# Kernel tuning notes

Measured on AMD Instinct MI355X. Metric: run time of the kernel, lower is better.

The kernel has to match this reference:

```python
import jax, jax.numpy as jnp
import numpy as np

INF = 1000000000.0
D = 1024


def setup_inputs() -> dict:
    key = jax.random.key(0)
    k_enc, k_r = jax.random.split(key)
    encoding = jax.random.normal(k_enc, (8, 2048, D), dtype=jnp.float32)
    R = jax.random.normal(k_r, (D, D), dtype=jnp.float32) / D  # init_with_zeros=False
    return {"encoding": encoding, "R": R}


def reference(encoding, R):
    b, n, d = encoding.shape
    # Q = encoding @ R ; scores = Q @ encoding^T  (bilinear relation attention)
    encR = jnp.einsum("bnd,de->bne", encoding, R)          # [b, n, d]
    scores = jnp.einsum("bnd,bmd->bnm", encR, encoding)     # [b, n, n]
    # causal mask: -INF above the diagonal (use_mask=True)
    mask = jnp.where(jnp.tril(jnp.ones((n, n), dtype=bool)), 0.0, -INF).astype(scores.dtype)
    A = jax.nn.softmax(scores + mask, axis=2)               # [b, n, n]
    return jnp.einsum("bnm,bmd->bnd", A, encoding)          # [b, n, d]
```

## Files before the change

### kernel.cpp

```cpp
#include <hip/hip_runtime.h>
#include <hip/hip_bf16.h>


typedef __attribute__((ext_vector_type(4))) float f32x4;
typedef __attribute__((ext_vector_type(4))) unsigned u32x4;
typedef __attribute__((ext_vector_type(8))) __fp16 f16x8;
typedef __attribute__((ext_vector_type(4))) __fp16 f16x4;
typedef __attribute__((ext_vector_type(2))) __fp16 f16x2;

#define MFMA16H(A, B, C) __builtin_amdgcn_mfma_f32_16x16x32_f16(A, B, C, 0, 0, 0)

__device__ __forceinline__ f16x4 cvt4h(f32x4 a) {
    union { f16x4 v; f16x2 h[2]; } r;
    r.h[0] = __builtin_amdgcn_cvt_pkrtz(a[0], a[1]);
    r.h[1] = __builtin_amdgcn_cvt_pkrtz(a[2], a[3]);
    return r.v;
}

__device__ __forceinline__ void gload16(const void* g, void* l) {
    __builtin_amdgcn_global_load_lds(
        (const __attribute__((address_space(1))) unsigned*)g,
        (__attribute__((address_space(3))) unsigned*)l, 16, 0, 0);
}

__global__ __launch_bounds__(256) void transpose_cvt_kernel(
    const float* __restrict__ src, __fp16* __restrict__ dstT,
    __fp16* __restrict__ dstH, int R, int C)
{
    __shared__ __align__(16) char lt[64 * 128];
    const int t = threadIdx.x;
    const int bz = blockIdx.z;
    const int r0 = blockIdx.x * 64, c0 = blockIdx.y * 64;
    const size_t so = (size_t)bz * R * C;
    const int tr = t >> 4;
    const int tc4 = (t & 15) * 4;
#pragma unroll
    for (int p = 0; p < 4; ++p) {
        int rl = tr + 16 * p;
        f32x4 x = *(const f32x4*)(src + so + (size_t)(r0 + rl) * C + c0 + tc4);
        f16x4 h = cvt4h(x);
        if (dstH) *(f16x4*)(dstH + so + (size_t)(r0 + rl) * C + c0 + tc4) = h;
        *(f16x4*)(lt + rl * 128 + ((tc4 * 2) ^ ((rl & 7) << 4))) = h;
    }
    __syncthreads();
#pragma unroll
    for (int p = 0; p < 4; ++p) {
        int dl = tr + 16 * p;
#pragma unroll
        for (int j = 0; j < 4; ++j) {
            int kl = (t & 15) + 16 * j;
            __fp16 v = *(const __fp16*)(lt + kl * 128 + ((dl * 2) ^ ((kl & 7) << 4)));
            dstT[so + (size_t)(c0 + dl) * R + r0 + kl] = v;
        }
    }
}

template <int CMODE>
__device__ __forceinline__ void gemm_core(
    const __fp16* __restrict__ A, const __fp16* __restrict__ B,
    char* __restrict__ Cptr, int ldA, int ldB, int ldC, int K, bool diag)
{
    __shared__ __align__(16) char sA[128 * 128];
    __shared__ __align__(16) char sB[128 * 128];
    const int t = threadIdx.x;
    const int w = t >> 6, l = t & 63;
    const int l15 = l & 15, lg = l >> 4;
    const int r0 = (w >> 1) * 64, c0 = (w & 1) * 64;
    const int swz = (l15 & 7) << 4;

    f32x4 acc[4][4];
#pragma unroll
    for (int i = 0; i < 4; ++i)
#pragma unroll
        for (int j = 0; j < 4; ++j) acc[i][j] = (f32x4){0.f, 0.f, 0.f, 0.f};

    const int strow = 32 * w + (l >> 3);
    const int gsrc = (((l & 7) ^ (l >> 3)) << 3);
    const __fp16* pa = A + (size_t)strow * ldA + gsrc;
    const __fp16* pb = B + (size_t)strow * ldB + gsrc;

    for (int kk = 0; kk < K; kk += 64) {
        __syncthreads();
#pragma unroll
        for (int i = 0; i < 4; ++i) {
            gload16(pa + (size_t)(8 * i) * ldA + kk, sA + w * 4096 + i * 1024);
            gload16(pb + (size_t)(8 * i) * ldB + kk, sB + w * 4096 + i * 1024);
        }
        __syncthreads();
#pragma unroll
        for (int ks = 0; ks < 2; ++ks) {
            f16x8 af[4], bf[4];
#pragma unroll
            for (int mt = 0; mt < 4; ++mt)
                af[mt] = *(const f16x8*)(sA + (r0 + 16 * mt + l15) * 128 + ((64 * ks + 16 * lg) ^ swz));
#pragma unroll
            for (int nt = 0; nt < 4; ++nt)
                bf[nt] = *(const f16x8*)(sB + (c0 + 16 * nt + l15) * 128 + ((64 * ks + 16 * lg) ^ swz));
#pragma unroll
            for (int mt = 0; mt < 4; ++mt)
#pragma unroll
                for (int nt = 0; nt < 4; ++nt)
                    acc[mt][nt] = MFMA16H(af[mt], bf[nt], acc[mt][nt]);
        }
    }
#pragma unroll
    for (int mt = 0; mt < 4; ++mt)
#pragma unroll
        for (int nt = 0; nt < 4; ++nt)
#pragma unroll
            for (int rg = 0; rg < 4; ++rg) {
                int rr = r0 + 16 * mt + 4 * lg + rg;
                int cc = c0 + 16 * nt + l15;
                float v = acc[mt][nt][rg];
                if (CMODE == 2) {
                    *(float*)(Cptr + ((size_t)rr * ldC + cc) * 4) = v;
                } else {
                    if (CMODE == 1 && diag && cc > rr) v = -30000.f;
                    *(__fp16*)(Cptr + ((size_t)rr * ldC + cc) * 2) = (__fp16)v;
                }
            }
}

__global__ __launch_bounds__(256) void gemm_qr(
    const __fp16* __restrict__ encH, const __fp16* __restrict__ Rt,
    __fp16* __restrict__ Qh)
{
    const int bm = ((int)blockIdx.x >> 3) * 128;
    const int bn = ((int)blockIdx.x & 7) * 128;
    gemm_core<0>(encH + (size_t)bm * 1024, Rt + (size_t)bn * 1024,
                 (char*)(Qh + (size_t)bm * 1024 + bn), 1024, 1024, 1024, 1024, false);
}

__global__ __launch_bounds__(256) void gemm_s(
    const __fp16* __restrict__ Qh, const __fp16* __restrict__ encH,
    __fp16* __restrict__ S)
{
    const int b = (int)blockIdx.x & 7;
    int rem = 135 - ((int)blockIdx.x >> 3);
    int qt = 0;
    while (rem > qt) { rem -= qt + 1; ++qt; }
    const int kt = rem;
    const size_t bo = (size_t)b * 2048 * 1024;
    const size_t so = (size_t)b * 2048 * 2048;
    gemm_core<1>(Qh + bo + (size_t)(qt * 128) * 1024,
                 encH + bo + (size_t)(kt * 128) * 1024,
                 (char*)(S + so + (size_t)(qt * 128) * 2048 + kt * 128),
                 1024, 1024, 2048, 1024, qt == kt);
}

__global__ __launch_bounds__(256) void gemm_pv(
    const __fp16* __restrict__ P, const __fp16* __restrict__ encT,
    float* __restrict__ out)
{
    const int b = (int)blockIdx.x & 7;
    const int r = (int)blockIdx.x >> 3;
    const int qtb = 15 - (r >> 3);
    const int dblk = r & 7;
    const size_t so = (size_t)b * 2048 * 2048;
    const size_t to = (size_t)b * 1024 * 2048;
    const int K = 128 * (qtb + 1);
    gemm_core<2>(P + so + (size_t)(qtb * 128) * 2048,
                 encT + to + (size_t)(dblk * 128) * 2048,
                 (char*)(out + (size_t)b * 2048 * 1024 + (size_t)(qtb * 128) * 1024 + dblk * 128),
                 2048, 2048, 1024, K, false);
}

__global__ __launch_bounds__(256) void softmax_kernel(__fp16* __restrict__ S)
{
    const int t = threadIdx.x;
    const int wv = t >> 6, l = t & 63;
    const int r = blockIdx.x * 4 + wv;
    const int b = blockIdx.y;
    __fp16* row = S + ((size_t)b * 2048 + r) * 2048;
    const int L = ((r >> 7) + 1) << 7;

    float v[4][8];
    float mx = -1e30f;
#pragma unroll
    for (int i = 0; i < 4; ++i) {
        int c0 = 8 * l + 512 * i;
        if (c0 < L) {
            f16x8 h = *reinterpret_cast<const f16x8*>(row + c0);
#pragma unroll
            for (int j = 0; j < 8; ++j) { v[i][j] = (float)h[j]; mx = fmaxf(mx, v[i][j]); }
        } else {
#pragma unroll
            for (int j = 0; j < 8; ++j) v[i][j] = -1e30f;
        }
    }
#pragma unroll
    for (int off = 1; off < 64; off <<= 1) mx = fmaxf(mx, __shfl_xor(mx, off));
    float sm = 0.f;
#pragma unroll
    for (int i = 0; i < 4; ++i)
#pragma unroll
        for (int j = 0; j < 8; ++j) { v[i][j] = __expf(v[i][j] - mx); sm += v[i][j]; }
#pragma unroll
    for (int off = 1; off < 64; off <<= 1) sm += __shfl_xor(sm, off);
    const float inv = 1.f / sm;
#pragma unroll
    for (int i = 0; i < 4; ++i) {
        int c0 = 8 * l + 512 * i;
        if (c0 < L) {
            union { f16x8 v8; f16x2 h[4]; } o;
#pragma unroll
            for (int j = 0; j < 4; ++j)
                o.h[j] = __builtin_amdgcn_cvt_pkrtz(v[i][2 * j] * inv, v[i][2 * j + 1] * inv);
            *reinterpret_cast<f16x8*>(row + c0) = o.v8;
        }
    }
}

__global__ __launch_bounds__(256) void qr_gemm_kernel(
    const float* __restrict__ A, const float* __restrict__ B, float* C)
{
    __shared__ __align__(16) char sA[128 * 64];
    __shared__ __align__(16) char sB[128 * 64];
    const int t = threadIdx.x;
    const int w = t >> 6, l = t & 63;
    const int l15 = l & 15, lg = l >> 4;
    const int bm = blockIdx.x * 128;
    const int bn = blockIdx.y * 128;

    f32x4 acc[4][4];
#pragma unroll
    for (int i = 0; i < 4; ++i)
#pragma unroll
        for (int j = 0; j < 4; ++j) acc[i][j] = (f32x4){0.f, 0.f, 0.f, 0.f};

    const int kq = 4 * (t & 7);
    const int i2 = t >> 3;

    for (int kk = 0; kk < 1024; kk += 32) {
#pragma unroll
        for (int it = 0; it < 4; ++it) {
            int m = i2 + 32 * it;
            f32x4 x = *reinterpret_cast<const f32x4*>(&A[(size_t)(bm + m) * 1024 + kk + kq]);
            *reinterpret_cast<f16x4*>(sA + m * 64 + ((2 * kq) ^ (((m >> 1) & 3) << 4))) = cvt4h(x);
        }
        {
            int n0 = 4 * i2;
            f32x4 x[4];
#pragma unroll
            for (int r = 0; r < 4; ++r)
                x[r] = *reinterpret_cast<const f32x4*>(&B[(size_t)(kk + kq + r) * 1024 + bn + n0]);
#pragma unroll
            for (int j = 0; j < 4; ++j) {
                int n = n0 + j;
                union { f16x4 v; f16x2 h[2]; } s;
                s.h[0] = __builtin_amdgcn_cvt_pkrtz(x[0][j], x[1][j]);
                s.h[1] = __builtin_amdgcn_cvt_pkrtz(x[2][j], x[3][j]);
                *reinterpret_cast<f16x4*>(sB + n * 64 + ((2 * kq) ^ (((n >> 1) & 3) << 4))) = s.v;
            }
        }
        __syncthreads();
        f16x8 af[4], bfv[4];
        const int r0 = (w >> 1) * 64, c0 = (w & 1) * 64;
#pragma unroll
        for (int mt = 0; mt < 4; ++mt) {
            int m = r0 + 16 * mt + l15;
            af[mt] = *reinterpret_cast<f16x8*>(sA + m * 64 + ((16 * lg) ^ (((m >> 1) & 3) << 4)));
        }
#pragma unroll
        for (int nt = 0; nt < 4; ++nt) {
            int n = c0 + 16 * nt + l15;
            bfv[nt] = *reinterpret_cast<f16x8*>(sB + n * 64 + ((16 * lg) ^ (((n >> 1) & 3) << 4)));
        }
#pragma unroll
        for (int mt = 0; mt < 4; ++mt)
#pragma unroll
            for (int nt = 0; nt < 4; ++nt)
                acc[mt][nt] = MFMA16H(af[mt], bfv[nt], acc[mt][nt]);
        __syncthreads();
    }
#pragma unroll
    for (int mt = 0; mt < 4; ++mt)
#pragma unroll
        for (int nt = 0; nt < 4; ++nt)
#pragma unroll
            for (int rg = 0; rg < 4; ++rg) {
                int row = bm + (w >> 1) * 64 + 16 * mt + 4 * lg + rg;
                int col = bn + (w & 1) * 64 + 16 * nt + l15;
                C[(size_t)row * 1024 + col] = acc[mt][nt][rg];
            }
}

__global__ __launch_bounds__(256) void s_gemm_kernel(
    const float* __restrict__ Q, const float* __restrict__ enc, __fp16* __restrict__ S)
{
    __shared__ __align__(16) char sA[128 * 64];
    __shared__ __align__(16) char sB[128 * 64];
    const int t = threadIdx.x;
    const int w = t >> 6, l = t & 63;
    const int l15 = l & 15, lg = l >> 4;

    int rem = 135 - (int)blockIdx.x;
    int qt = 0;
    while (rem > qt) { rem -= qt + 1; ++qt; }
    const int kt = rem;
    const int b = blockIdx.y;
    const float* Arow = Q + ((size_t)b * 2048 + qt * 128) * 1024;
    const float* Brow = enc + ((size_t)b * 2048 + kt * 128) * 1024;

    f32x4 acc[4][4];
#pragma unroll
    for (int i = 0; i < 4; ++i)
#pragma unroll
        for (int j = 0; j < 4; ++j) acc[i][j] = (f32x4){0.f, 0.f, 0.f, 0.f};

    const int kq = 4 * (t & 7);
    const int i2 = t >> 3;

    for (int kk = 0; kk < 1024; kk += 32) {
#pragma unroll
        for (int it = 0; it < 4; ++it) {
            int m = i2 + 32 * it;
            int sw = (2 * kq) ^ (((m >> 1) & 3) << 4);
            f32x4 xa = *reinterpret_cast<const f32x4*>(&Arow[(size_t)m * 1024 + kk + kq]);
            f32x4 xb = *reinterpret_cast<const f32x4*>(&Brow[(size_t)m * 1024 + kk + kq]);
            *reinterpret_cast<f16x4*>(sA + m * 64 + sw) = cvt4h(xa);
            *reinterpret_cast<f16x4*>(sB + m * 64 + sw) = cvt4h(xb);
        }
        __syncthreads();
        f16x8 af[4], bfv[4];
        const int r0 = (w >> 1) * 64, c0 = (w & 1) * 64;
#pragma unroll
        for (int mt = 0; mt < 4; ++mt) {
            int m = r0 + 16 * mt + l15;
            af[mt] = *reinterpret_cast<f16x8*>(sA + m * 64 + ((16 * lg) ^ (((m >> 1) & 3) << 4)));
        }
#pragma unroll
        for (int nt = 0; nt < 4; ++nt) {
            int n = c0 + 16 * nt + l15;
            bfv[nt] = *reinterpret_cast<f16x8*>(sB + n * 64 + ((16 * lg) ^ (((n >> 1) & 3) << 4)));
        }
#pragma unroll
        for (int mt = 0; mt < 4; ++mt)
#pragma unroll
            for (int nt = 0; nt < 4; ++nt)
                acc[mt][nt] = MFMA16H(af[mt], bfv[nt], acc[mt][nt]);
        __syncthreads();
    }
    const int r0 = (w >> 1) * 64, c0 = (w & 1) * 64;
#pragma unroll
    for (int mt = 0; mt < 4; ++mt)
#pragma unroll
        for (int nt = 0; nt < 4; ++nt)
#pragma unroll
            for (int rg = 0; rg < 4; ++rg) {
                int rt = r0 + 16 * mt + 4 * lg + rg;
                int ct = c0 + 16 * nt + l15;
                float v = acc[mt][nt][rg];
                if (kt == qt && ct > rt) v = -30000.f;
                S[((size_t)b * 2048 + qt * 128 + rt) * 2048 + kt * 128 + ct] = (__fp16)v;
            }
}

__global__ __launch_bounds__(512) void pv_gemm_kernel(
    const __fp16* __restrict__ P, const float* __restrict__ enc, float* __restrict__ out)
{
    __shared__ __align__(16) char sA[128 * 128];
    __shared__ __align__(16) char sB[128 * 128];
    const int t = threadIdx.x;
    const int w = t >> 6, l = t & 63;
    const int l15 = l & 15, lg = (l >> 4) & 3;
    const int wq = w >> 2, wdv = w & 3;
    const int qtb = 15 - (int)blockIdx.x;
    const int dblk = blockIdx.y;
    const int b = blockIdx.z;
    const int q0 = 128 * qtb;
    const int nkv = 128 * (qtb + 1);
    const __fp16* Pbase = P + ((size_t)b * 2048 + q0) * 2048;
    const float* Eb = enc + (size_t)b * 2048 * 1024;

    f32x4 acc[4][2];
#pragma unroll
    for (int i = 0; i < 4; ++i)
#pragma unroll
        for (int j = 0; j < 2; ++j) acc[i][j] = (f32x4){0.f, 0.f, 0.f, 0.f};

    const int ar = t >> 2, aseg = t & 3;
    const int ba = t >> 5, bdq = t & 31;

    for (int kv0 = 0; kv0 < nkv; kv0 += 64) {
        __syncthreads();
        {
            const __fp16* src = Pbase + (size_t)ar * 2048 + kv0 + 16 * aseg;
            u32x4 v0 = *reinterpret_cast<const u32x4*>(src);
            u32x4 v1 = *reinterpret_cast<const u32x4*>(src + 8);
            const int sw = (ar & 7) << 4;
            *reinterpret_cast<u32x4*>(sA + ar * 128 + ((32 * aseg) ^ sw)) = v0;
            *reinterpret_cast<u32x4*>(sA + ar * 128 + ((32 * aseg + 16) ^ sw)) = v1;
        }
        {
            const float* src = Eb + (size_t)(kv0 + 4 * ba) * 1024 + 128 * dblk + 4 * bdq;
            f32x4 x0 = *reinterpret_cast<const f32x4*>(src);
            f32x4 x1 = *reinterpret_cast<const f32x4*>(src + 1024);
            f32x4 x2 = *reinterpret_cast<const f32x4*>(src + 2048);
            f32x4 x3 = *reinterpret_cast<const f32x4*>(src + 3072);
#pragma unroll
            for (int j = 0; j < 4; ++j) {
                int d = 4 * bdq + j;
                union { f16x4 v; f16x2 h[2]; } s;
                s.h[0] = __builtin_amdgcn_cvt_pkrtz(x0[j], x1[j]);
                s.h[1] = __builtin_amdgcn_cvt_pkrtz(x2[j], x3[j]);
                *reinterpret_cast<f16x4*>(sB + d * 128 + ((8 * ba) ^ ((d & 7) << 4))) = s.v;
            }
        }
        __syncthreads();
#pragma unroll
        for (int ks = 0; ks < 2; ++ks) {
            f16x8 afr[4], bfr[2];
#pragma unroll
            for (int mt = 0; mt < 4; ++mt) {
                int rr = 64 * wq + 16 * mt + l15;
                afr[mt] = *reinterpret_cast<f16x8*>(sA + rr * 128 + ((64 * ks + 16 * lg) ^ ((rr & 7) << 4)));
            }
#pragma unroll
            for (int nt = 0; nt < 2; ++nt) {
                int d = 32 * wdv + 16 * nt + l15;
                bfr[nt] = *reinterpret_cast<f16x8*>(sB + d * 128 + ((64 * ks + 16 * lg) ^ ((d & 7) << 4)));
            }
#pragma unroll
            for (int mt = 0; mt < 4; ++mt)
#pragma unroll
                for (int nt = 0; nt < 2; ++nt)
                    acc[mt][nt] = MFMA16H(afr[mt], bfr[nt], acc[mt][nt]);
        }
    }
#pragma unroll
    for (int mt = 0; mt < 4; ++mt)
#pragma unroll
        for (int nt = 0; nt < 2; ++nt)
#pragma unroll
            for (int rg = 0; rg < 4; ++rg) {
                size_t row = (size_t)b * 2048 + q0 + 64 * wq + 16 * mt + 4 * lg + rg;
                int col = 128 * dblk + 32 * wdv + 16 * nt + l15;
                out[row * 1024 + col] = acc[mt][nt][rg];
            }
}

extern "C" void kernel_launch(void* const* d_in, const int* in_sizes, int n_in,
                              void* d_out, int out_size, void* d_ws, size_t ws_size,
                              hipStream_t stream)
{
    const float* enc = (const float*)d_in[0];
    const float* R = (const float*)d_in[1];
    float* out = (float*)d_out;
    const size_t MB = 1u << 20;

    if (ws_size >= 98 * MB) {
        __fp16* S = (__fp16*)d_ws;
        __fp16* encT = (__fp16*)((char*)d_ws + 64 * MB);
        __fp16* Rt = (__fp16*)((char*)d_ws + 96 * MB);
        __fp16* Qh = (__fp16*)d_out;
        __fp16* encH = (__fp16*)d_out + (size_t)16384 * 1024;

        transpose_cvt_kernel<<<dim3(32, 16, 8), 256, 0, stream>>>(enc, encT, encH, 2048, 1024);
        transpose_cvt_kernel<<<dim3(16, 16, 1), 256, 0, stream>>>(R, Rt, (__fp16*)nullptr, 1024, 1024);
        gemm_qr<<<dim3(1024), 256, 0, stream>>>(encH, Rt, Qh);
        gemm_s<<<dim3(1088), 256, 0, stream>>>(Qh, encH, S);
        softmax_kernel<<<dim3(512, 8), 256, 0, stream>>>(S);
        gemm_pv<<<dim3(1024), 256, 0, stream>>>(S, encT, out);
    } else {
        __fp16* S = (__fp16*)d_ws;
        qr_gemm_kernel<<<dim3(128, 8), 256, 0, stream>>>(enc, R, out);
        s_gemm_kernel<<<dim3(136, 8), 256, 0, stream>>>(out, enc, S);
        softmax_kernel<<<dim3(512, 8), 256, 0, stream>>>(S);
        pv_gemm_kernel<<<dim3(16, 8, 8), 512, 0, stream>>>(S, enc, out);
    }
}
```

Before: 191.2 us.

## Replace Q=enc@R GEMM with 256x256-tile, 8-wave, double-buffered pipelined kernel

Adds a dedicated gemm_qr256 kernel that computes each 256x256 output tile with 512 threads and 128KB of LDS. It double-buffers K-slices with direct global-to-LDS loads interleaved between MFMA groups, using explicit waitcnt, barriers and setprio. The larger tile raises arithmetic intensity and should hide load latency in the QR projection GEMM. In exchange it launches only 256 blocks, which may underfill the GPU, and it depends on hand-tuned waitcnt ordering being correct.

```diff
diff --git a/kernel.cpp b/kernel.cpp
--- a/kernel.cpp
+++ b/kernel.cpp
@@ -22,6 +22,10 @@
         (const __attribute__((address_space(1))) unsigned*)g,
         (__attribute__((address_space(3))) unsigned*)l, 16, 0, 0);
 }
+
+#define BAR() do { __builtin_amdgcn_sched_barrier(0); \
+                   __builtin_amdgcn_s_barrier();      \
+                   __builtin_amdgcn_sched_barrier(0); } while (0)
 
 __global__ __launch_bounds__(256) void transpose_cvt_kernel(
     const float* __restrict__ src, __fp16* __restrict__ dstT,
@@ -53,6 +57,128 @@
             dstT[so + (size_t)(c0 + dl) * R + r0 + kl] = v;
         }
     }
+}
+
+__global__ __launch_bounds__(512, 2) void gemm_qr256(
+    const __fp16* __restrict__ encH, const __fp16* __restrict__ Rt,
+    __fp16* __restrict__ Qh)
+{
+    __shared__ __align__(16) char lds[131072];
+    const int t = threadIdx.x;
+    const int w = t >> 6, l = t & 63;
+    const int l15 = l & 15, lg = (l >> 4) & 3;
+    const int wr = w >> 2, wc = w & 3;
+    const int bm = ((int)blockIdx.x >> 2) * 256;
+    const int bn = ((int)blockIdx.x & 3) * 256;
+    const __fp16* Ag = encH + (size_t)bm * 1024;
+    const __fp16* Bg = Rt + (size_t)bn * 1024;
+
+    const int srow = 32 * w + (l >> 2);
+    const int slg = ((l & 3) - ((l >> 3) & 3)) & 3;
+    const int slotr = ((l >> 4) + ((l & 15) >> 1)) & 3;
+
+    f32x4 acc[8][4];
+#pragma unroll
+    for (int i = 0; i < 8; ++i)
+#pragma unroll
+        for (int j = 0; j < 4; ++j) acc[i][j] = (f32x4){0.f, 0.f, 0.f, 0.f};
+
+    auto stage = [&](int op, int tile, int kh) {
+        const __fp16* src = (op ? Bg : Ag) + (size_t)srow * 1024 + tile * 64 + kh * 32 + slg * 8;
+        char* dst = lds + (tile & 1) * 65536 + op * 32768 + kh * 16384 + w * 2048;
+        gload16(src, dst);
+        gload16(src + (size_t)16 * 1024, dst + 1024);
+    };
+    auto rdA = [&](int buf, int ks, int mf) {
+        return *(const f16x8*)(lds + buf * 65536 + ks * 16384
+                               + (128 * wr + 16 * mf + l15) * 64 + slotr * 16);
+    };
+    auto rdB = [&](int buf, int ks, int nf) {
+        return *(const f16x8*)(lds + buf * 65536 + 32768 + ks * 16384
+                               + (64 * wc + 16 * nf + l15) * 64 + slotr * 16);
+    };
+
+    stage(0, 0, 0); stage(1, 0, 0); stage(0, 0, 1); stage(1, 0, 1);
+    stage(0, 1, 0); stage(1, 1, 0);
+
+    f16x8 afr[4], bfr[4];
+
+#define MF16(mbase)                                                     \
+    __builtin_amdgcn_s_setprio(1);                                      \
+    _Pragma("unroll") for (int mf = 0; mf < 4; ++mf)                    \
+        _Pragma("unroll") for (int nf = 0; nf < 4; ++nf)                \
+            acc[(mbase) + mf][nf] = MFMA16H(afr[mf], bfr[nf], acc[(mbase) + mf][nf]); \
+    __builtin_amdgcn_s_setprio(0);
+
+    for (int i = 0; i < 8; ++i) {
+        const bool lastI = (i == 7);
+        asm volatile("s_waitcnt vmcnt(8)" ::: "memory");
+        BAR();
+#pragma unroll
+        for (int nf = 0; nf < 4; ++nf) bfr[nf] = rdB(0, 0, nf);
+#pragma unroll
+        for (int mf = 0; mf < 4; ++mf) afr[mf] = rdA(0, 0, mf);
+        stage(0, 2 * i + 1, 1);
+        MF16(0)
+        BAR();
+#pragma unroll
+        for (int mf = 0; mf < 4; ++mf) afr[mf] = rdA(0, 0, mf + 4);
+        stage(1, 2 * i + 1, 1);
+        MF16(4)
+        asm volatile("s_waitcnt vmcnt(8)" ::: "memory");
+        BAR();
+#pragma unroll
+        for (int nf = 0; nf < 4; ++nf) bfr[nf] = rdB(0, 1, nf);
+#pragma unroll
+        for (int mf = 0; mf < 4; ++mf) afr[mf] = rdA(0, 1, mf);
+        if (!lastI) stage(0, 2 * i + 2, 0);
+        MF16(0)
+        BAR();
+#pragma unroll
+        for (int mf = 0; mf < 4; ++mf) afr[mf] = rdA(0, 1, mf + 4);
+        if (!lastI) stage(1, 2 * i + 2, 0);
+        MF16(4)
+        if (!lastI) asm volatile("s_waitcnt vmcnt(8)" ::: "memory");
+        else        asm volatile("s_waitcnt vmcnt(4)" ::: "memory");
+        BAR();
+#pragma unroll
+        for (int nf = 0; nf < 4; ++nf) bfr[nf] = rdB(1, 0, nf);
+#pragma unroll
+        for (int mf = 0; mf < 4; ++mf) afr[mf] = rdA(1, 0, mf);
+        if (!lastI) stage(0, 2 * i + 2, 1);
+        MF16(0)
+        BAR();
+#pragma unroll
+        for (int mf = 0; mf < 4; ++mf) afr[mf] = rdA(1, 0, mf + 4);
+        if (!lastI) stage(1, 2 * i + 2, 1);
+        MF16(4)
+        if (!lastI) asm volatile("s_waitcnt vmcnt(8)" ::: "memory");
+        else        asm volatile("s_waitcnt vmcnt(0)" ::: "memory");
+        BAR();
+#pragma unroll
+        for (int nf = 0; nf < 4; ++nf) bfr[nf] = rdB(1, 1, nf);
+#pragma unroll
+        for (int mf = 0; mf < 4; ++mf) afr[mf] = rdA(1, 1, mf);
+        if (!lastI) stage(0, 2 * i + 3, 0);
+        MF16(0)
+        BAR();
+#pragma unroll
+        for (int mf = 0; mf < 4; ++mf) afr[mf] = rdA(1, 1, mf + 4);
+        if (!lastI) stage(1, 2 * i + 3, 0);
+        MF16(4)
+    }
+#undef MF16
+
+#pragma unroll
+    for (int mf = 0; mf < 8; ++mf)
+#pragma unroll
+        for (int nf = 0; nf < 4; ++nf)
+#pragma unroll
+            for (int rg = 0; rg < 4; ++rg) {
+                int rr = bm + 128 * wr + 16 * mf + 4 * lg + rg;
+                int cc = bn + 64 * wc + 16 * nf + l15;
+                Qh[(size_t)rr * 1024 + cc] = (__fp16)acc[mf][nf][rg];
+            }
 }
 
 template <int CMODE>
@@ -119,16 +245,6 @@
                     *(__fp16*)(Cptr + ((size_t)rr * ldC + cc) * 2) = (__fp16)v;
                 }
             }
-}
-
-__global__ __launch_bounds__(256) void gemm_qr(
-    const __fp16* __restrict__ encH, const __fp16* __restrict__ Rt,
-    __fp16* __restrict__ Qh)
-{
-    const int bm = ((int)blockIdx.x >> 3) * 128;
-    const int bn = ((int)blockIdx.x & 7) * 128;
-    gemm_core<0>(encH + (size_t)bm * 1024, Rt + (size_t)bn * 1024,
-                 (char*)(Qh + (size_t)bm * 1024 + bn), 1024, 1024, 1024, 1024, false);
 }
 
 __global__ __launch_bounds__(256) void gemm_s(
@@ -458,7 +574,7 @@
 
         transpose_cvt_kernel<<<dim3(32, 16, 8), 256, 0, stream>>>(enc, encT, encH, 2048, 1024);
         transpose_cvt_kernel<<<dim3(16, 16, 1), 256, 0, stream>>>(R, Rt, (__fp16*)nullptr, 1024, 1024);
-        gemm_qr<<<dim3(1024), 256, 0, stream>>>(encH, Rt, Qh);
+        gemm_qr256<<<dim3(256), 512, 0, stream>>>(encH, Rt, Qh);
         gemm_s<<<dim3(1088), 256, 0, stream>>>(Qh, encH, S);
         softmax_kernel<<<dim3(512, 8), 256, 0, stream>>>(S);
         gemm_pv<<<dim3(1024), 256, 0, stream>>>(S, encT, out);
```

New measurement: 183.3 us. 4.1% less time.
